# Kernel tuning notes

Hardware: AMD Instinct MI355X
Metric: run time of the kernel (lower is better)

The kernel has to match this reference:

```python
import jax, jax.numpy as jnp
from jax import lax
import numpy as np

# correlation hyperparams (from init_kwargs)
MAX_D = 32      # maxDisplacement
PAD = 1         # zero padding
K = 3           # patch (kernel) size
STRIDE_K = 1    # stride over output pixels
STRIDE_D = 1    # stride over displacements


def setup_inputs() -> dict:
    key = jax.random.key(0)
    k0, k1 = jax.random.split(key)
    x0 = jax.random.normal(k0, (4, 64, 256, 512), dtype=jnp.float32)
    x1 = jax.random.normal(k1, (4, 64, 256, 512), dtype=jnp.float32)
    return {"x0": x0, "x1": x1}


def _corr2d(x0, x1):
    # x0, x1: [B, C, H, W] NCHW feature maps
    B, C, H, W = x0.shape
    # zero-pad spatially; x1 gets extra width padding so all displacements are in-bounds
    x0p = jnp.pad(x0, ((0, 0), (0, 0), (PAD, PAD), (PAD, PAD)))
    x1p = jnp.pad(x1, ((0, 0), (0, 0), (PAD, PAD), (PAD + MAX_D, PAD + MAX_D)))
    Wp = W + 2 * PAD
    # width offsets into x1p for displacements d = -MAX_D .. MAX_D step STRIDE_D
    offsets = jnp.arange(0, 2 * MAX_D + 1, STRIDE_D, dtype=jnp.int32)

    def step(carry, off):
        x1s = lax.dynamic_slice_in_dim(x1p, off, Wp, axis=3)   # [B,C,Hp,Wp]
        prod = jnp.sum(x0p * x1s, axis=1)                      # channel dot -> [B,Hp,Wp]
        # KxK box-sum over the patch, stride STRIDE_K -> [B,Ho,Wo]
        s = lax.reduce_window(prod, jnp.float32(0), lax.add,
                              (1, K, K), (1, STRIDE_K, STRIDE_K), 'VALID')
        return carry, s

    _, out = lax.scan(step, None, offsets)        # [nD, B, Ho, Wo]
    out = jnp.transpose(out, (1, 0, 2, 3))        # [B, nD, Ho, Wo]
    return out / jnp.asarray(K * K * C, out.dtype)


def reference(x0, x1):
    return _corr2d(x0, x1)
```

## Files before the change

### kernel.cpp

```cpp
#include <hip/hip_runtime.h>

#define WF 512
#define HF 256
#define CF 64
#define NDTOT 65
#define DP 72

static constexpr size_t CH  = (size_t)HF * WF;
static constexpr size_t WH  = (size_t)HF * WF;
static constexpr float  INV = 1.0f / 576.0f;

typedef _Float16 f16;
typedef _Float16 f16x8 __attribute__((ext_vector_type(8)));
typedef float    f32x4 __attribute__((ext_vector_type(4)));

__global__ __launch_bounds__(256)
void corr_gram(const float* __restrict__ x0, const float* __restrict__ x1,
               f16* __restrict__ ws) {
    const int f = blockIdx.x;
    const int xcd = f & 7;
    const int strip = (f >> 3) & 3;
    const int pl = f >> 5;
    const int pair = xcd * 128 + pl;
    const int y = pair & 255;
    const int b = pair >> 8;

    const int t = threadIdx.x;
    const int l = t & 63;
    const int w = t >> 6;
    const int xs = strip << 7;
    const int jb = xs - 32;

    const int n  = l & 15;
    const int ks = (l >> 4) * 8;

    const float* x0r = x0 + (size_t)b * CF * CH + (size_t)y * WF;
    const float* x1r = x1 + (size_t)b * CF * CH + (size_t)y * WF;

    const int colA = xs + 2 * w * 16 + n;

    f32x4 acc[10];
#pragma unroll
    for (int i = 0; i < 10; ++i) acc[i] = (f32x4)0.0f;

#pragma unroll
    for (int hh = 0; hh < 2; ++hh) {
        const size_t cb = (size_t)(hh * 32 + ks) * CH;

        float ar0[8], ar1[8];
        const float* pA = x0r + cb + colA;
#pragma unroll
        for (int i = 0; i < 8; ++i) ar0[i] = pA[(size_t)i * CH];
#pragma unroll
        for (int i = 0; i < 8; ++i) ar1[i] = pA[(size_t)i * CH + 16];
        f16x8 ah0, ah1, al0, al1;
#pragma unroll
        for (int i = 0; i < 8; ++i) {
            const f16 h0 = (f16)ar0[i]; ah0[i] = h0; al0[i] = (f16)(ar0[i] - (float)h0);
            const f16 h1 = (f16)ar1[i]; ah1[i] = h1; al1[i] = (f16)(ar1[i] - (float)h1);
        }

#pragma unroll
        for (int g2 = 0; g2 < 2; ++g2) {
            float br[3][8];
#pragma unroll
            for (int k3 = 0; k3 < 3; ++k3) {
                const int jt = 2 * w + 3 * g2 + k3;
                const int j = jb + jt * 16 + n;
                const bool ok = (unsigned)j < (unsigned)WF;
                const float* pB = x1r + cb + j;
#pragma unroll
                for (int i = 0; i < 8; ++i)
                    br[k3][i] = ok ? pB[(size_t)i * CH] : 0.f;
            }
            f16x8 bh[3], bl[3];
#pragma unroll
            for (int k3 = 0; k3 < 3; ++k3)
#pragma unroll
                for (int i = 0; i < 8; ++i) {
                    const f16 h = (f16)br[k3][i];
                    bh[k3][i] = h;
                    bl[k3][i] = (f16)(br[k3][i] - (float)h);
                }

#define TRIPLE(ai, AH, AL, bi) \
    do { \
        acc[ai] = __builtin_amdgcn_mfma_f32_16x16x32_f16(AH, bh[bi], acc[ai], 0, 0, 0); \
        acc[ai] = __builtin_amdgcn_mfma_f32_16x16x32_f16(AH, bl[bi], acc[ai], 0, 0, 0); \
        acc[ai] = __builtin_amdgcn_mfma_f32_16x16x32_f16(AL, bh[bi], acc[ai], 0, 0, 0); \
    } while (0)

            if (g2 == 0) {
                TRIPLE(0, ah0, al0, 0);
                TRIPLE(1, ah0, al0, 1);
                TRIPLE(2, ah0, al0, 2);
                TRIPLE(5, ah1, al1, 1);
                TRIPLE(6, ah1, al1, 2);
            } else {
                TRIPLE(3, ah0, al0, 0);
                TRIPLE(4, ah0, al0, 1);
                TRIPLE(7, ah1, al1, 0);
                TRIPLE(8, ah1, al1, 1);
                TRIPLE(9, ah1, al1, 2);
            }
#undef TRIPLE
        }
    }

    f16* wsrow = ws + ((size_t)(b * HF + y) * WF) * DP;
#pragma unroll
    for (int xtl = 0; xtl < 2; ++xtl) {
#pragma unroll
        for (int p = 0; p < 5; ++p) {
            const int i = xtl * 5 + p;
#pragma unroll
            for (int q = 0; q < 4; ++q) {
                const int m = (l >> 4) * 4 + q;
                const int x = xs + (2 * w + xtl) * 16 + m;
                const int d = 16 * p + n - m;
                if ((unsigned)d < (unsigned)NDTOT)
                    wsrow[(size_t)x * DP + d] = (f16)acc[i][q];
            }
        }
    }
}

__global__ __launch_bounds__(256)
void corr_box(const f16* __restrict__ ws, float* __restrict__ out) {
    const int xt = blockIdx.x;
    const int yt = blockIdx.y;
    const int b = blockIdx.z;
    const int t = threadIdx.x;
    const int x0b = xt * 32, y0 = yt * 8;

    __shared__ f16 S[10 * 34][DP];

    for (int u = 0; u < 10; ++u) {
        const int yy = y0 - 1 + u;
        const bool yok = (unsigned)yy < (unsigned)HF;
        const f16* src = ws + ((size_t)(b * HF + yy) * WF + (x0b - 1)) * DP;
#pragma unroll
        for (int sub = 0; sub < 2; ++sub) {
            const int idx = sub * 256 + t;
            if (idx < 306) {
                const int v = idx / 9, dg = idx - v * 9;
                const int xx = x0b - 1 + v;
                f16x8 val;
#pragma unroll
                for (int jj = 0; jj < 8; ++jj) val[jj] = (f16)0.f;
                if (yok && (unsigned)xx < (unsigned)WF)
                    val = *(const f16x8*)(src + (size_t)v * DP + dg * 8);
                *(f16x8*)&S[u * 34 + v][dg * 8] = val;
            }
        }
    }
    __syncthreads();

    const int ly = t >> 5, lx = t & 31;
    const int yg = y0 + ly, xg = x0b + lx;
    float* o0 = out + (size_t)b * NDTOT * WH + (size_t)yg * WF + xg;

#pragma unroll 1
    for (int dg = 0; dg < 9; ++dg) {
        f16x8 s;
#pragma unroll
        for (int jj = 0; jj < 8; ++jj) s[jj] = (f16)0.f;
#pragma unroll
        for (int du = 0; du < 3; ++du)
#pragma unroll
            for (int dv = 0; dv < 3; ++dv)
                s += *(const f16x8*)&S[(ly + du) * 34 + (lx + dv)][dg * 8];
#pragma unroll
        for (int jj = 0; jj < 8; ++jj) {
            const int d = dg * 8 + jj;
            if (d < NDTOT) o0[(size_t)d * WH] = (float)s[jj] * INV;
        }
    }
}

__global__ void corr_naive(const float* __restrict__ x0, const float* __restrict__ x1,
                           float* __restrict__ out) {
    const size_t total = (size_t)4 * NDTOT * WH;
    size_t idx = (size_t)blockIdx.x * blockDim.x + threadIdx.x;
    if (idx >= total) return;
    const int j = (int)(idx % WF);
    const int i = (int)((idx / WF) % HF);
    const int d = (int)((idx / WH) % NDTOT);
    const int b = (int)(idx / ((size_t)NDTOT * WH));
    const int disp = d - 32;
    float s = 0.f;
    for (int u = i - 1; u <= i + 1; ++u) {
        if (u < 0 || u >= HF) continue;
        for (int v = j - 1; v <= j + 1; ++v) {
            if (v < 0 || v >= WF) continue;
            const int v1c = v + disp;
            if (v1c < 0 || v1c >= WF) continue;
            const float* p0 = x0 + (size_t)b * CF * CH + (size_t)u * WF + v;
            const float* p1 = x1 + (size_t)b * CF * CH + (size_t)u * WF + v1c;
            for (int c = 0; c < CF; ++c)
                s += p0[(size_t)c * CH] * p1[(size_t)c * CH];
        }
    }
    out[idx] = s * INV;
}

extern "C" void kernel_launch(void* const* d_in, const int* in_sizes, int n_in,
                              void* d_out, int out_size, void* d_ws, size_t ws_size,
                              hipStream_t stream) {
    const float* x0 = (const float*)d_in[0];
    const float* x1 = (const float*)d_in[1];
    float* out = (float*)d_out;

    const size_t wsNeed = (size_t)4 * HF * WF * DP * sizeof(f16);

    if (ws_size >= wsNeed) {
        f16* ws = (f16*)d_ws;
        corr_gram<<<dim3(4096), dim3(256), 0, stream>>>(x0, x1, ws);
        corr_box<<<dim3(16, 32, 4), dim3(256), 0, stream>>>(ws, out);
    } else {
        const size_t total = (size_t)4 * NDTOT * WH;
        const int blocks = (int)((total + 255) / 256);
        corr_naive<<<dim3(blocks), dim3(256), 0, stream>>>(x0, x1, out);
    }
}
```

Measured before the change: 155.5 us.

## Stage gram-kernel operands through LDS via async global_load_lds

Rewrites the corr_gram main loop so each block copies its x0 and x1 channel tiles into shared memory with 16-byte async global-to-LDS loads, using XOR-swizzled layouts. Fragments are then read from LDS rather than by strided per-lane global loads, and each x1 column is converted to f16 hi/lo once and reused across the two A tiles. The goal is to replace scattered 4-byte global reads with coalesced wide transfers and cut redundant B loads. In exchange it adds 40 KB of LDS per block, barriers between the two channel halves, and a launch-bounds occupancy hint.

Result: faster. 136.9 us (-12.0%).

```diff
diff --git a/kernel.cpp b/kernel.cpp
--- a/kernel.cpp
+++ b/kernel.cpp
@@ -14,7 +14,10 @@
 typedef _Float16 f16x8 __attribute__((ext_vector_type(8)));
 typedef float    f32x4 __attribute__((ext_vector_type(4)));
 
-__global__ __launch_bounds__(256)
+typedef __attribute__((address_space(3))) void lds_void_t;
+typedef const __attribute__((address_space(1))) void glb_void_t;
+
+__global__ __launch_bounds__(256, 4)
 void corr_gram(const float* __restrict__ x0, const float* __restrict__ x1,
                f16* __restrict__ ws) {
     const int f = blockIdx.x;
@@ -31,81 +34,106 @@
     const int xs = strip << 7;
     const int jb = xs - 32;
 
-    const int n  = l & 15;
-    const int ks = (l >> 4) * 8;
+    const int n   = l & 15;
+    const int n4  = n >> 2, nr = n & 3;
+    const int ksl = (l >> 4) * 8;
+    const int qs  = ((l >> 4) & 3) << 2;
+
+    __shared__ float lds[10240];
 
     const float* x0r = x0 + (size_t)b * CF * CH + (size_t)y * WF;
     const float* x1r = x1 + (size_t)b * CF * CH + (size_t)y * WF;
 
-    const int colA = xs + 2 * w * 16 + n;
+    int o0[4], o1[6];
+#pragma unroll
+    for (int qi = 0; qi < 4; ++qi) {
+        const int P = qi * 256 + t;
+        const int L = P ^ (((P >> 8) & 3) << 2);
+        o0[qi] = (L >> 5) * (int)CH + xs + 4 * (L & 31);
+    }
+#pragma unroll
+    for (int ri = 0; ri < 6; ++ri) {
+        const int P = ri * 256 + t;
+        const int c = P / 48;
+        const int j4 = (P - 48 * c) ^ (((c >> 3) & 3) << 2);
+        int jg = jb + 4 * j4;
+        jg = jg < 0 ? 0 : (jg > 508 ? 508 : jg);
+        o1[ri] = c * (int)CH + jg;
+    }
+
+    const int A0b = (ksl * 32 + ((8 * w + n4) ^ qs)) * 4 + nr;
+    const int A1b = (ksl * 32 + ((8 * w + 4 + n4) ^ qs)) * 4 + nr;
+    int Bb[6];
+#pragma unroll
+    for (int jt = 0; jt < 6; ++jt)
+        Bb[jt] = 4096 + (48 * ksl + ((8 * w + 4 * jt + n4) ^ qs)) * 4 + nr;
 
     f32x4 acc[10];
 #pragma unroll
     for (int i = 0; i < 10; ++i) acc[i] = (f32x4)0.0f;
 
-#pragma unroll
-    for (int hh = 0; hh < 2; ++hh) {
-        const size_t cb = (size_t)(hh * 32 + ks) * CH;
-
-        float ar0[8], ar1[8];
-        const float* pA = x0r + cb + colA;
-#pragma unroll
-        for (int i = 0; i < 8; ++i) ar0[i] = pA[(size_t)i * CH];
-#pragma unroll
-        for (int i = 0; i < 8; ++i) ar1[i] = pA[(size_t)i * CH + 16];
-        f16x8 ah0, ah1, al0, al1;
-#pragma unroll
-        for (int i = 0; i < 8; ++i) {
-            const f16 h0 = (f16)ar0[i]; ah0[i] = h0; al0[i] = (f16)(ar0[i] - (float)h0);
-            const f16 h1 = (f16)ar1[i]; ah1[i] = h1; al1[i] = (f16)(ar1[i] - (float)h1);
-        }
-
-#pragma unroll
-        for (int g2 = 0; g2 < 2; ++g2) {
-            float br[3][8];
-#pragma unroll
-            for (int k3 = 0; k3 < 3; ++k3) {
-                const int jt = 2 * w + 3 * g2 + k3;
-                const int j = jb + jt * 16 + n;
-                const bool ok = (unsigned)j < (unsigned)WF;
-                const float* pB = x1r + cb + j;
-#pragma unroll
-                for (int i = 0; i < 8; ++i)
-                    br[k3][i] = ok ? pB[(size_t)i * CH] : 0.f;
-            }
-            f16x8 bh[3], bl[3];
-#pragma unroll
-            for (int k3 = 0; k3 < 3; ++k3)
-#pragma unroll
-                for (int i = 0; i < 8; ++i) {
-                    const f16 h = (f16)br[k3][i];
-                    bh[k3][i] = h;
-                    bl[k3][i] = (f16)(br[k3][i] - (float)h);
-                }
-
-#define TRIPLE(ai, AH, AL, bi) \
+#define TRIPLE(ai, AH, AL) \
     do { \
-        acc[ai] = __builtin_amdgcn_mfma_f32_16x16x32_f16(AH, bh[bi], acc[ai], 0, 0, 0); \
-        acc[ai] = __builtin_amdgcn_mfma_f32_16x16x32_f16(AH, bl[bi], acc[ai], 0, 0, 0); \
-        acc[ai] = __builtin_amdgcn_mfma_f32_16x16x32_f16(AL, bh[bi], acc[ai], 0, 0, 0); \
+        acc[ai] = __builtin_amdgcn_mfma_f32_16x16x32_f16(AH, bh, acc[ai], 0, 0, 0); \
+        acc[ai] = __builtin_amdgcn_mfma_f32_16x16x32_f16(AH, bl, acc[ai], 0, 0, 0); \
+        acc[ai] = __builtin_amdgcn_mfma_f32_16x16x32_f16(AL, bh, acc[ai], 0, 0, 0); \
     } while (0)
 
-            if (g2 == 0) {
-                TRIPLE(0, ah0, al0, 0);
-                TRIPLE(1, ah0, al0, 1);
-                TRIPLE(2, ah0, al0, 2);
-                TRIPLE(5, ah1, al1, 1);
-                TRIPLE(6, ah1, al1, 2);
-            } else {
-                TRIPLE(3, ah0, al0, 0);
-                TRIPLE(4, ah0, al0, 1);
-                TRIPLE(7, ah1, al1, 0);
-                TRIPLE(8, ah1, al1, 1);
-                TRIPLE(9, ah1, al1, 2);
-            }
+#pragma unroll
+    for (int h = 0; h < 2; ++h) {
+        const size_t hb = (size_t)h * 32 * CH;
+#pragma unroll
+        for (int qi = 0; qi < 4; ++qi)
+            __builtin_amdgcn_global_load_lds(
+                (glb_void_t*)(x0r + hb + o0[qi]),
+                (lds_void_t*)(lds + (qi * 256 + w * 64) * 4), 16, 0, 0);
+#pragma unroll
+        for (int ri = 0; ri < 6; ++ri)
+            __builtin_amdgcn_global_load_lds(
+                (glb_void_t*)(x1r + hb + o1[ri]),
+                (lds_void_t*)(lds + 4096 + (ri * 256 + w * 64) * 4), 16, 0, 0);
+
+        __syncthreads();
+
+        f16x8 ah0, al0, ah1, al1;
+        {
+            float ar[8];
+#pragma unroll
+            for (int i = 0; i < 8; ++i) ar[i] = lds[A0b + i * 128];
+#pragma unroll
+            for (int i = 0; i < 8; ++i) {
+                const f16 hv = (f16)ar[i];
+                ah0[i] = hv; al0[i] = (f16)(ar[i] - (float)hv);
+            }
+#pragma unroll
+            for (int i = 0; i < 8; ++i) ar[i] = lds[A1b + i * 128];
+#pragma unroll
+            for (int i = 0; i < 8; ++i) {
+                const f16 hv = (f16)ar[i];
+                ah1[i] = hv; al1[i] = (f16)(ar[i] - (float)hv);
+            }
+        }
+
+#pragma unroll
+        for (int jt = 0; jt < 6; ++jt) {
+            float br[8];
+#pragma unroll
+            for (int i = 0; i < 8; ++i) br[i] = lds[Bb[jt] + i * 192];
+            const bool okB = (unsigned)(jb + (2 * w + jt) * 16 + n) < (unsigned)WF;
+            f16x8 bh, bl;
+#pragma unroll
+            for (int i = 0; i < 8; ++i) {
+                const float v = okB ? br[i] : 0.f;
+                const f16 hv = (f16)v;
+                bh[i] = hv; bl[i] = (f16)(v - (float)hv);
+            }
+            if (jt < 5) TRIPLE(jt, ah0, al0);
+            if (jt >= 1) TRIPLE(4 + jt, ah1, al1);
+        }
+
+        if (h == 0) __syncthreads();
+    }
 #undef TRIPLE
-        }
-    }
 
     f16* wsrow = ws + ((size_t)(b * HF + y) * WF) * DP;
 #pragma unroll
```

## Stage gram inputs through swizzled LDS with K-loop prefetch and coalesced stores

Applied to the files above, without the earlier changes.

Reworks corr_gram so each wave owns a 32-column strip. Input channels are loaded from global memory with coalesced accesses into a swizzled LDS tile, and the next K chunk is software-prefetched into registers. The kernel now uses 16x16x16 MFMA fragments with an fp16 hi/lo split. Results are staged in LDS, padding is zeroed, and each row is written to the workspace with 16-byte vector stores instead of scattered f16 stores. This targets uncoalesced global loads and stores, at the cost of extra LDS traffic, more MFMA instructions per K, and an occupancy hint of 4.

Measured after the change: 134.0 us. 13.8% less time.

```diff
diff --git a/kernel.cpp b/kernel.cpp
--- a/kernel.cpp
+++ b/kernel.cpp
@@ -11,117 +11,165 @@
 static constexpr float  INV = 1.0f / 576.0f;
 
 typedef _Float16 f16;
+typedef _Float16 f16x4 __attribute__((ext_vector_type(4)));
 typedef _Float16 f16x8 __attribute__((ext_vector_type(8)));
 typedef float    f32x4 __attribute__((ext_vector_type(4)));
 
-__global__ __launch_bounds__(256)
+#if __has_builtin(__builtin_amdgcn_mfma_f32_16x16x16f16)
+#define MFMA16(A, B, C) __builtin_amdgcn_mfma_f32_16x16x16f16((A), (B), (C), 0, 0, 0)
+#define FRAG_T f16x4
+__device__ __forceinline__ f16x4 mkfrag(f16 a, f16 b, f16 c, f16 d) {
+    f16x4 r; r[0] = a; r[1] = b; r[2] = c; r[3] = d; return r;
+}
+#else
+#define MFMA16(A, B, C) __builtin_amdgcn_mfma_f32_16x16x32_f16((A), (B), (C), 0, 0, 0)
+#define FRAG_T f16x8
+__device__ __forceinline__ f16x8 mkfrag(f16 a, f16 b, f16 c, f16 d) {
+    f16x8 r; r[0] = a; r[1] = b; r[2] = c; r[3] = d;
+    r[4] = (f16)0.f; r[5] = (f16)0.f; r[6] = (f16)0.f; r[7] = (f16)0.f; return r;
+}
+#endif
+
+__global__ __launch_bounds__(256, 4)
 void corr_gram(const float* __restrict__ x0, const float* __restrict__ x1,
                f16* __restrict__ ws) {
     const int f = blockIdx.x;
-    const int xcd = f & 7;
-    const int strip = (f >> 3) & 3;
-    const int pl = f >> 5;
-    const int pair = xcd * 128 + pl;
-    const int y = pair & 255;
-    const int b = pair >> 8;
+    const int tid = (f & 7) * 512 + (f >> 3);
+    const int b = tid >> 10;
+    const int y = (tid >> 2) & 255;
+    const int sg = tid & 3;
 
     const int t = threadIdx.x;
     const int l = t & 63;
     const int w = t >> 6;
-    const int xs = strip << 7;
+    const int xs = (sg * 4 + w) * 32;
     const int jb = xs - 32;
 
     const int n  = l & 15;
-    const int ks = (l >> 4) * 8;
+    const int kq = l >> 4;
+    const int sn = (n & 3) ^ (n >> 2);
+
+    __shared__ float lds[8192];
+    float* base = lds + w * 2048;
 
     const float* x0r = x0 + (size_t)b * CF * CH + (size_t)y * WF;
     const float* x1r = x1 + (size_t)b * CF * CH + (size_t)y * WF;
 
-    const int colA = xs + 2 * w * 16 + n;
+    const int c0 = l & 31, qa = l >> 5;
+    const int sA = (c0 & 3) ^ ((c0 >> 2) & 3);
+    int aoff[2], awad[2];
+    aoff[0] = (4 * qa) * (int)CH + xs + c0;
+    aoff[1] = (4 * (qa + 2)) * (int)CH + xs + c0;
+    awad[0] = c0 * 16 + 4 * (qa ^ sA);
+    awad[1] = c0 * 16 + 4 * ((qa + 2) ^ sA);
+    int boff[6], bwad[6];
+#pragma unroll
+    for (int u = 0; u < 6; ++u) {
+        const int v = u * 64 + l;
+        const int q = v / 96;
+        const int cb = v - 96 * q;
+        int jg = jb + cb;
+        jg = jg < 0 ? 0 : (jg > 511 ? 511 : jg);
+        boff[u] = (4 * q) * (int)CH + jg;
+        bwad[u] = 512 + cb * 16 + 4 * (q ^ ((cb & 3) ^ ((cb >> 2) & 3)));
+    }
+
+    int ard[2], brd[6];
+#pragma unroll
+    for (int xt = 0; xt < 2; ++xt) ard[xt] = (16 * xt + n) * 16 + 4 * (kq ^ sn);
+#pragma unroll
+    for (int jt = 0; jt < 6; ++jt) brd[jt] = 512 + (16 * jt + n) * 16 + 4 * (kq ^ sn);
+    bool okj[6];
+#pragma unroll
+    for (int jt = 0; jt < 6; ++jt) okj[jt] = (unsigned)(jb + 16 * jt + n) < (unsigned)WF;
 
     f32x4 acc[10];
 #pragma unroll
     for (int i = 0; i < 10; ++i) acc[i] = (f32x4)0.0f;
 
-#pragma unroll
-    for (int hh = 0; hh < 2; ++hh) {
-        const size_t cb = (size_t)(hh * 32 + ks) * CH;
-
-        float ar0[8], ar1[8];
-        const float* pA = x0r + cb + colA;
-#pragma unroll
-        for (int i = 0; i < 8; ++i) ar0[i] = pA[(size_t)i * CH];
-#pragma unroll
-        for (int i = 0; i < 8; ++i) ar1[i] = pA[(size_t)i * CH + 16];
-        f16x8 ah0, ah1, al0, al1;
-#pragma unroll
-        for (int i = 0; i < 8; ++i) {
-            const f16 h0 = (f16)ar0[i]; ah0[i] = h0; al0[i] = (f16)(ar0[i] - (float)h0);
-            const f16 h1 = (f16)ar1[i]; ah1[i] = h1; al1[i] = (f16)(ar1[i] - (float)h1);
-        }
-
-#pragma unroll
-        for (int g2 = 0; g2 < 2; ++g2) {
-            float br[3][8];
-#pragma unroll
-            for (int k3 = 0; k3 < 3; ++k3) {
-                const int jt = 2 * w + 3 * g2 + k3;
-                const int j = jb + jt * 16 + n;
-                const bool ok = (unsigned)j < (unsigned)WF;
-                const float* pB = x1r + cb + j;
-#pragma unroll
-                for (int i = 0; i < 8; ++i)
-                    br[k3][i] = ok ? pB[(size_t)i * CH] : 0.f;
-            }
-            f16x8 bh[3], bl[3];
-#pragma unroll
-            for (int k3 = 0; k3 < 3; ++k3)
-#pragma unroll
-                for (int i = 0; i < 8; ++i) {
-                    const f16 h = (f16)br[k3][i];
-                    bh[k3][i] = h;
-                    bl[k3][i] = (f16)(br[k3][i] - (float)h);
-                }
-
-#define TRIPLE(ai, AH, AL, bi) \
-    do { \
-        acc[ai] = __builtin_amdgcn_mfma_f32_16x16x32_f16(AH, bh[bi], acc[ai], 0, 0, 0); \
-        acc[ai] = __builtin_amdgcn_mfma_f32_16x16x32_f16(AH, bl[bi], acc[ai], 0, 0, 0); \
-        acc[ai] = __builtin_amdgcn_mfma_f32_16x16x32_f16(AL, bh[bi], acc[ai], 0, 0, 0); \
+    float ra[8], rb[24];
+#define LOADK(kk) do { const int kb = 16 * (kk) * (int)CH; \
+    _Pragma("unroll") for (int j = 0; j < 2; ++j) \
+    _Pragma("unroll") for (int i = 0; i < 4; ++i) ra[4*j+i] = x0r[aoff[j] + kb + i * (int)CH]; \
+    _Pragma("unroll") for (int u = 0; u < 6; ++u) \
+    _Pragma("unroll") for (int i = 0; i < 4; ++i) rb[4*u+i] = x1r[boff[u] + kb + i * (int)CH]; \
     } while (0)
 
-            if (g2 == 0) {
-                TRIPLE(0, ah0, al0, 0);
-                TRIPLE(1, ah0, al0, 1);
-                TRIPLE(2, ah0, al0, 2);
-                TRIPLE(5, ah1, al1, 1);
-                TRIPLE(6, ah1, al1, 2);
-            } else {
-                TRIPLE(3, ah0, al0, 0);
-                TRIPLE(4, ah0, al0, 1);
-                TRIPLE(7, ah1, al1, 0);
-                TRIPLE(8, ah1, al1, 1);
-                TRIPLE(9, ah1, al1, 2);
-            }
+#define TRIPLE(ai, AH, AL) do { \
+    acc[ai] = MFMA16(AH, bh, acc[ai]); \
+    acc[ai] = MFMA16(AH, bl, acc[ai]); \
+    acc[ai] = MFMA16(AL, bh, acc[ai]); } while (0)
+
+    LOADK(0);
+
+#pragma unroll 1
+    for (int kk = 0; kk < 4; ++kk) {
+#pragma unroll
+        for (int j = 0; j < 2; ++j)
+            *(float4*)&base[awad[j]] = make_float4(ra[4*j], ra[4*j+1], ra[4*j+2], ra[4*j+3]);
+#pragma unroll
+        for (int u = 0; u < 6; ++u)
+            *(float4*)&base[bwad[u]] = make_float4(rb[4*u], rb[4*u+1], rb[4*u+2], rb[4*u+3]);
+
+        if (kk < 3) LOADK(kk + 1);
+
+        FRAG_T ah[2], al[2];
+#pragma unroll
+        for (int xt = 0; xt < 2; ++xt) {
+            const float4 fa = *(const float4*)&base[ard[xt]];
+            const float tmp[4] = {fa.x, fa.y, fa.z, fa.w};
+            f16 h0 = (f16)tmp[0], h1 = (f16)tmp[1], h2 = (f16)tmp[2], h3 = (f16)tmp[3];
+            ah[xt] = mkfrag(h0, h1, h2, h3);
+            al[xt] = mkfrag((f16)(tmp[0] - (float)h0), (f16)(tmp[1] - (float)h1),
+                            (f16)(tmp[2] - (float)h2), (f16)(tmp[3] - (float)h3));
+        }
+#pragma unroll
+        for (int jt = 0; jt < 6; ++jt) {
+            const float4 fb = *(const float4*)&base[brd[jt]];
+            float tmp[4] = {fb.x, fb.y, fb.z, fb.w};
+#pragma unroll
+            for (int i = 0; i < 4; ++i) tmp[i] = okj[jt] ? tmp[i] : 0.f;
+            f16 h0 = (f16)tmp[0], h1 = (f16)tmp[1], h2 = (f16)tmp[2], h3 = (f16)tmp[3];
+            const FRAG_T bh = mkfrag(h0, h1, h2, h3);
+            const FRAG_T bl = mkfrag((f16)(tmp[0] - (float)h0), (f16)(tmp[1] - (float)h1),
+                                     (f16)(tmp[2] - (float)h2), (f16)(tmp[3] - (float)h3));
+            if (jt < 5)  TRIPLE(jt, ah[0], al[0]);
+            if (jt >= 1) TRIPLE(4 + jt, ah[1], al[1]);
+        }
+    }
 #undef TRIPLE
-        }
-    }
-
-    f16* wsrow = ws + ((size_t)(b * HF + y) * WF) * DP;
-#pragma unroll
-    for (int xtl = 0; xtl < 2; ++xtl) {
+#undef LOADK
+
+    f16* eb = (f16*)base;
+#pragma unroll
+    for (int xt = 0; xt < 2; ++xt) {
 #pragma unroll
         for (int p = 0; p < 5; ++p) {
-            const int i = xtl * 5 + p;
+            const int i = xt * 5 + p;
 #pragma unroll
             for (int q = 0; q < 4; ++q) {
-                const int m = (l >> 4) * 4 + q;
-                const int x = xs + (2 * w + xtl) * 16 + m;
+                const int m = kq * 4 + q;
+                const int xl = xt * 16 + m;
                 const int d = 16 * p + n - m;
                 if ((unsigned)d < (unsigned)NDTOT)
-                    wsrow[(size_t)x * DP + d] = (f16)acc[i][q];
+                    eb[xl * DP + d] = (f16)acc[i][q];
             }
         }
+    }
+#pragma unroll
+    for (int i = 0; i < 4; ++i) {
+        const int idx = l + 64 * i;
+        if (idx < 224) {
+            const int xl = idx / 7;
+            eb[xl * DP + NDTOT + (idx - 7 * xl)] = (f16)0.f;
+        }
+    }
+    uint4* dst = (uint4*)(ws + ((size_t)(b * HF + y) * WF + xs) * DP);
+    const uint4* src = (const uint4*)eb;
+#pragma unroll
+    for (int i = 0; i < 5; ++i) {
+        const int idx = l + 64 * i;
+        if (idx < 288) dst[idx] = src[idx];
     }
 }
 
```

## Stage gram inputs through LDS, drop split-f16 MFMA, coalesce workspace writes

Applied to the files above, without the earlier changes.

The gram kernel now loads x0/x1 tiles with vectorized float4 global loads, converts them to f16 and stages them in shared memory, then each wave reads its MFMA fragments from LDS. Loading of the second channel half is overlapped with compute on the first. The hi/lo split-precision triple MFMA is replaced by a single f16 MFMA, cutting matrix work to a third but lowering accuracy. Results are assembled in LDS and written to the workspace as coalesced 16-byte stores, with pad entries zeroed.

Result: faster. 129.7 us (-16.6%).

```diff
diff --git a/kernel.cpp b/kernel.cpp
--- a/kernel.cpp
+++ b/kernel.cpp
@@ -5,16 +5,19 @@
 #define CF 64
 #define NDTOT 65
 #define DP 72
+#define APAD 40
 
 static constexpr size_t CH  = (size_t)HF * WF;
 static constexpr size_t WH  = (size_t)HF * WF;
 static constexpr float  INV = 1.0f / 576.0f;
 
 typedef _Float16 f16;
+typedef _Float16 f16x2 __attribute__((ext_vector_type(2)));
+typedef _Float16 f16x4 __attribute__((ext_vector_type(4)));
 typedef _Float16 f16x8 __attribute__((ext_vector_type(8)));
 typedef float    f32x4 __attribute__((ext_vector_type(4)));
 
-__global__ __launch_bounds__(256)
+__global__ __launch_bounds__(256, 2)
 void corr_gram(const float* __restrict__ x0, const float* __restrict__ x1,
                f16* __restrict__ ws) {
     const int f = blockIdx.x;
@@ -28,100 +31,126 @@
     const int t = threadIdx.x;
     const int l = t & 63;
     const int w = t >> 6;
-    const int xs = strip << 7;
-    const int jb = xs - 32;
+    const int X0 = strip << 7;
+    const int jb = X0 - 32;
 
     const int n  = l & 15;
-    const int ks = (l >> 4) * 8;
+    const int kq = l >> 4;
+
+    __shared__ f16 S[12800];
+    f16* SA = S;
+    f16* SB = S + 5120;
 
     const float* x0r = x0 + (size_t)b * CF * CH + (size_t)y * WF;
     const float* x1r = x1 + (size_t)b * CF * CH + (size_t)y * WF;
 
-    const int colA = xs + 2 * w * 16 + n;
+    const int c4  = t & 31;
+    const int chq = t >> 5;
+    int bchp[3], bc4b[3], bcol[3]; bool bok[3];
+#pragma unroll
+    for (int u = 0; u < 3; ++u) {
+        const int idx = u * 256 + t;
+        bchp[u] = idx / 48;
+        bc4b[u] = idx - 48 * bchp[u];
+        bcol[u] = jb + 4 * bc4b[u];
+        bok[u]  = (unsigned)bcol[u] < (unsigned)WF;
+    }
+
+#define LOADH(h, A4, B4) do { \
+    const float* xa = x0r + (size_t)((h) * 32 + 4 * chq) * CH + (X0 + 4 * c4); \
+    _Pragma("unroll") \
+    for (int j = 0; j < 4; ++j) A4[j] = *(const f32x4*)(xa + (size_t)j * CH); \
+    _Pragma("unroll") \
+    for (int u = 0; u < 3; ++u) { \
+        const float* xb = x1r + (size_t)((h) * 32 + 2 * bchp[u]) * CH + bcol[u]; \
+        B4[2*u]     = bok[u] ? *(const f32x4*)xb        : (f32x4)0.f; \
+        B4[2*u + 1] = bok[u] ? *(const f32x4*)(xb + CH) : (f32x4)0.f; \
+    } \
+} while (0)
+
+#define CVTW(A4, B4) do { \
+    _Pragma("unroll") \
+    for (int j2 = 0; j2 < 4; ++j2) { \
+        f16x4 v; \
+        v[0] = (f16)A4[0][j2]; v[1] = (f16)A4[1][j2]; \
+        v[2] = (f16)A4[2][j2]; v[3] = (f16)A4[3][j2]; \
+        *(f16x4*)&SA[(4 * c4 + j2) * APAD + 4 * chq] = v; \
+    } \
+    _Pragma("unroll") \
+    for (int u = 0; u < 3; ++u) { \
+        _Pragma("unroll") \
+        for (int j2 = 0; j2 < 4; ++j2) { \
+            f16x2 v; \
+            v[0] = (f16)B4[2*u][j2]; v[1] = (f16)B4[2*u + 1][j2]; \
+            *(f16x2*)&SB[(4 * bc4b[u] + j2) * APAD + 2 * bchp[u]] = v; \
+        } \
+    } \
+} while (0)
+
+#define COMP() do { \
+    const f16x8 a0 = *(const f16x8*)&SA[(w * 32 + n) * APAD + kq * 8]; \
+    const f16x8 a1 = *(const f16x8*)&SA[(w * 32 + 16 + n) * APAD + kq * 8]; \
+    _Pragma("unroll") \
+    for (int jt = 0; jt < 6; ++jt) { \
+        const f16x8 bf = *(const f16x8*)&SB[(w * 32 + jt * 16 + n) * APAD + kq * 8]; \
+        if (jt < 5) \
+            acc[jt] = __builtin_amdgcn_mfma_f32_16x16x32_f16(a0, bf, acc[jt], 0, 0, 0); \
+        if (jt >= 1) \
+            acc[4 + jt] = __builtin_amdgcn_mfma_f32_16x16x32_f16(a1, bf, acc[4 + jt], 0, 0, 0); \
+    } \
+} while (0)
 
     f32x4 acc[10];
 #pragma unroll
     for (int i = 0; i < 10; ++i) acc[i] = (f32x4)0.0f;
 
-#pragma unroll
-    for (int hh = 0; hh < 2; ++hh) {
-        const size_t cb = (size_t)(hh * 32 + ks) * CH;
-
-        float ar0[8], ar1[8];
-        const float* pA = x0r + cb + colA;
-#pragma unroll
-        for (int i = 0; i < 8; ++i) ar0[i] = pA[(size_t)i * CH];
-#pragma unroll
-        for (int i = 0; i < 8; ++i) ar1[i] = pA[(size_t)i * CH + 16];
-        f16x8 ah0, ah1, al0, al1;
-#pragma unroll
-        for (int i = 0; i < 8; ++i) {
-            const f16 h0 = (f16)ar0[i]; ah0[i] = h0; al0[i] = (f16)(ar0[i] - (float)h0);
-            const f16 h1 = (f16)ar1[i]; ah1[i] = h1; al1[i] = (f16)(ar1[i] - (float)h1);
-        }
-
-#pragma unroll
-        for (int g2 = 0; g2 < 2; ++g2) {
-            float br[3][8];
-#pragma unroll
-            for (int k3 = 0; k3 < 3; ++k3) {
-                const int jt = 2 * w + 3 * g2 + k3;
-                const int j = jb + jt * 16 + n;
-                const bool ok = (unsigned)j < (unsigned)WF;
-                const float* pB = x1r + cb + j;
-#pragma unroll
-                for (int i = 0; i < 8; ++i)
-                    br[k3][i] = ok ? pB[(size_t)i * CH] : 0.f;
-            }
-            f16x8 bh[3], bl[3];
-#pragma unroll
-            for (int k3 = 0; k3 < 3; ++k3)
-#pragma unroll
-                for (int i = 0; i < 8; ++i) {
-                    const f16 h = (f16)br[k3][i];
-                    bh[k3][i] = h;
-                    bl[k3][i] = (f16)(br[k3][i] - (float)h);
-                }
-
-#define TRIPLE(ai, AH, AL, bi) \
-    do { \
-        acc[ai] = __builtin_amdgcn_mfma_f32_16x16x32_f16(AH, bh[bi], acc[ai], 0, 0, 0); \
-        acc[ai] = __builtin_amdgcn_mfma_f32_16x16x32_f16(AH, bl[bi], acc[ai], 0, 0, 0); \
-        acc[ai] = __builtin_amdgcn_mfma_f32_16x16x32_f16(AL, bh[bi], acc[ai], 0, 0, 0); \
-    } while (0)
-
-            if (g2 == 0) {
-                TRIPLE(0, ah0, al0, 0);
-                TRIPLE(1, ah0, al0, 1);
-                TRIPLE(2, ah0, al0, 2);
-                TRIPLE(5, ah1, al1, 1);
-                TRIPLE(6, ah1, al1, 2);
-            } else {
-                TRIPLE(3, ah0, al0, 0);
-                TRIPLE(4, ah0, al0, 1);
-                TRIPLE(7, ah1, al1, 0);
-                TRIPLE(8, ah1, al1, 1);
-                TRIPLE(9, ah1, al1, 2);
-            }
-#undef TRIPLE
-        }
-    }
-
-    f16* wsrow = ws + ((size_t)(b * HF + y) * WF) * DP;
-#pragma unroll
-    for (int xtl = 0; xtl < 2; ++xtl) {
+    f32x4 a4[4], b4[6], a4n[4], b4n[6];
+
+    LOADH(0, a4, b4);
+    CVTW(a4, b4);
+    __syncthreads();
+    LOADH(1, a4n, b4n);
+    COMP();
+    __syncthreads();
+    CVTW(a4n, b4n);
+    __syncthreads();
+    COMP();
+    __syncthreads();
+
+#undef COMP
+#undef CVTW
+#undef LOADH
+
+    f16* eb = S + w * 2304;
+#pragma unroll
+    for (int xt = 0; xt < 2; ++xt) {
 #pragma unroll
         for (int p = 0; p < 5; ++p) {
-            const int i = xtl * 5 + p;
+            const int i = xt * 5 + p;
 #pragma unroll
             for (int q = 0; q < 4; ++q) {
-                const int m = (l >> 4) * 4 + q;
-                const int x = xs + (2 * w + xtl) * 16 + m;
+                const int m = kq * 4 + q;
+                const int xl = xt * 16 + m;
                 const int d = 16 * p + n - m;
                 if ((unsigned)d < (unsigned)NDTOT)
-                    wsrow[(size_t)x * DP + d] = (f16)acc[i][q];
+                    eb[xl * DP + d] = (f16)acc[i][q];
             }
         }
+    }
+#pragma unroll
+    for (int i = 0; i < 4; ++i) {
+        const int idx = l + 64 * i;
+        if (idx < 224) {
+            const int xl = idx / 7;
+            eb[xl * DP + NDTOT + (idx - 7 * xl)] = (f16)0.f;
+        }
+    }
+    uint4* dst = (uint4*)(ws + ((size_t)(b * HF + y) * WF + X0 + w * 32) * DP);
+    const uint4* src = (const uint4*)eb;
+#pragma unroll
+    for (int i = 0; i < 5; ++i) {
+        const int idx = l + 64 * i;
+        if (idx < 288) dst[idx] = src[idx];
     }
 }
 
```
